# Performance work log

Measured on AMD Instinct MI355X. Metric: run time of the kernel, lower is better.

The kernel has to match this reference:

```python
import jax, jax.numpy as jnp
import numpy as np

B, L, D, NH, NV, T = 4096, 5, 128, 16, 4, 100
NUM_USERS = NUM_ITEMS = 100000
FC1_DIM = NV * D + NH * sum(L - l + 1 for l in range(1, L + 1))  # 752


def setup_inputs() -> dict:
    key = jax.random.key(0)
    ks = jax.random.split(key, 12)
    s = 0.02
    return {
        "seq": jax.random.randint(ks[0], (B, L), 0, NUM_ITEMS),
        "user": jax.random.randint(ks[1], (B,), 0, NUM_USERS),
        "items": jax.random.randint(ks[2], (B, T), 0, NUM_ITEMS),
        "item_table": jax.random.normal(ks[3], (NUM_ITEMS, D), jnp.float32) * s,
        "user_table": jax.random.normal(ks[4], (NUM_USERS, D), jnp.float32) * s,
        "Wv": jax.random.normal(ks[5], (NV, L), jnp.float32) * s,
        "bv": jnp.zeros((NV,), jnp.float32),
        "Wh": jax.random.normal(ks[6], (L, NH, L, D), jnp.float32) * s,
        "bh": jnp.zeros((L, NH), jnp.float32),
        "W1": jax.random.normal(ks[7], (FC1_DIM, D), jnp.float32) * s,
        "b1": jnp.zeros((D,), jnp.float32),
        "W2_table": jax.random.normal(ks[8], (NUM_ITEMS, 2 * D), jnp.float32) * s,
        "b2_table": jnp.zeros((NUM_ITEMS, 1), jnp.float32),
        "_predict": 1,
    }


def reference(seq, user, items, item_table, user_table, Wv, bv, Wh, bh, W1, b1, W2_table, b2_table, _predict):
    emb = item_table[seq]            # (B, L, D)
    uemb = user_table[user]          # (B, D)

    # vertical conv: kernel (L,1), nv out channels -> (B, NV, D), flattened
    ver = jnp.einsum("btd,vt->bvd", emb, Wv) + bv[None, :, None]
    ver_flat = ver.reshape(B, NV * D)

    # horizontal convs: for each kernel length l, NH filters of shape (l, D)
    hor = []
    for l in range(1, L + 1):
        lout = L - l + 1
        # windows: (B, lout, l, D) built from l shifted views
        win = jnp.stack([emb[:, s:s + lout] for s in range(l)], axis=2)
        h = jnp.einsum("btsd,fsd->bft", win, Wh[l - 1, :, :l]) + bh[l - 1][None, :, None]
        hor.append(jax.nn.relu(h).reshape(B, NH * lout))

    z = jnp.concatenate([ver_flat] + hor, axis=1)      # (B, FC1_DIM)
    x = jax.nn.relu(z @ W1 + b1)                        # (B, D)
    xc = jnp.concatenate([x, uemb], axis=1)             # (B, 2D)

    w2 = W2_table[items]                                # (B, T, 2D)
    b2 = b2_table[items][..., 0]                        # (B, T)
    res = jnp.einsum("btd,bd->bt", w2, xc) + b2
    return res
```

## Files before the change

### kernel.cpp

```cpp
#include <hip/hip_runtime.h>


constexpr int Bsz  = 4096;
constexpr int Lq   = 5;
constexpr int Dd   = 128;
constexpr int NHh  = 16;
constexpr int NVv  = 4;
constexpr int Tt   = 100;
constexpr int FC1  = 752;
constexpr int G    = 4;
constexpr int NTHR = 256;

__global__ __launch_bounds__(NTHR, 4) void caser_fused(
    const int* __restrict__ seq, const int* __restrict__ user,
    const int* __restrict__ items,
    const float* __restrict__ item_table, const float* __restrict__ user_table,
    const float* __restrict__ Wv, const float* __restrict__ bv,
    const float* __restrict__ Wh, const float* __restrict__ bh,
    const float* __restrict__ W1, const float* __restrict__ b1,
    const float* __restrict__ W2_table, const float* __restrict__ b2_table,
    float* __restrict__ out)
{
    __shared__ float emb[G][Lq * Dd];
    __shared__ float z[G][FC1];
    __shared__ float xc[G][2 * Dd];
    __shared__ int   s_items[G * Tt];
    __shared__ float s_b2[G * Tt];
    __shared__ float s_res[G * Tt];

    const int tid = threadIdx.x;
    const int b0  = blockIdx.x * G;

    for (int idx = tid; idx < G * Tt; idx += NTHR) {
        int it = items[b0 * Tt + idx];
        s_items[idx] = it;
        s_b2[idx]    = b2_table[it];
    }

    for (int idx = tid; idx < G * Lq * Dd; idx += NTHR) {
        int gt  = idx >> 7;
        int d   = idx & (Dd - 1);
        int row = seq[b0 * Lq + gt];
        emb[0][idx] = item_table[row * Dd + d];
    }
    for (int idx = tid; idx < G * Dd; idx += NTHR) {
        int g = idx >> 7, d = idx & (Dd - 1);
        xc[g][Dd + d] = user_table[user[b0 + g] * Dd + d];
    }
    __syncthreads();

    for (int idx = tid; idx < G * NVv * Dd; idx += NTHR) {
        int g = idx >> 9;
        int v = (idx >> 7) & 3;
        int d = idx & (Dd - 1);
        float acc = bv[v];
        #pragma unroll
        for (int t = 0; t < Lq; ++t)
            acc = fmaf(emb[g][t * Dd + d], Wv[v * Lq + t], acc);
        z[g][v * Dd + d] = acc;
    }

    if (tid < 240) {
        int glt = tid >> 4, f = tid & 15;
        int l, t;
        if      (glt < 5)  { l = 1; t = glt; }
        else if (glt < 9)  { l = 2; t = glt - 5; }
        else if (glt < 12) { l = 3; t = glt - 9; }
        else if (glt < 14) { l = 4; t = glt - 12; }
        else               { l = 5; t = 0; }
        const int lout = Lq - l + 1;
        const int zoff = (l == 1) ? 0 : (l == 2) ? 80 : (l == 3) ? 144
                       : (l == 4) ? 192 : 224;
        float acc[G];
        {
            float bias = bh[(l - 1) * NHh + f];
            #pragma unroll
            for (int g = 0; g < G; ++g) acc[g] = bias;
        }
        for (int s = 0; s < l; ++s) {
            const float4* w4 = reinterpret_cast<const float4*>(
                Wh + (((l - 1) * NHh + f) * Lq + s) * Dd);
            const int ebase = (t + s) * Dd;
            #pragma unroll 4
            for (int d4 = 0; d4 < Dd / 4; ++d4) {
                float4 w = w4[d4];
                #pragma unroll
                for (int g = 0; g < G; ++g) {
                    float4 e = *reinterpret_cast<const float4*>(
                        &emb[g][ebase + d4 * 4]);
                    acc[g] = fmaf(e.x, w.x,
                             fmaf(e.y, w.y,
                             fmaf(e.z, w.z,
                             fmaf(e.w, w.w, acc[g]))));
                }
            }
        }
        #pragma unroll
        for (int g = 0; g < G; ++g)
            z[g][NVv * Dd + zoff + f * lout + t] = fmaxf(acc[g], 0.0f);
    }
    __syncthreads();

    float* part = &emb[0][0];
    {
        int j = tid & (Dd - 1);
        int half = tid >> 7;
        float acc[G] = {0.f, 0.f, 0.f, 0.f};
        const float* w1p = W1 + j;
        int i0 = half * (FC1 / 2);
        for (int i = i0; i < i0 + FC1 / 2; i += 4) {
            float4 zz[G];
            #pragma unroll
            for (int g = 0; g < G; ++g)
                zz[g] = *reinterpret_cast<const float4*>(&z[g][i]);
            float w0 = w1p[(i + 0) * Dd];
            float w1 = w1p[(i + 1) * Dd];
            float w2 = w1p[(i + 2) * Dd];
            float w3 = w1p[(i + 3) * Dd];
            #pragma unroll
            for (int g = 0; g < G; ++g)
                acc[g] = fmaf(zz[g].x, w0,
                         fmaf(zz[g].y, w1,
                         fmaf(zz[g].z, w2,
                         fmaf(zz[g].w, w3, acc[g]))));
        }
        #pragma unroll
        for (int g = 0; g < G; ++g)
            part[(half * G + g) * Dd + j] = acc[g];
    }
    __syncthreads();
    if (tid < Dd) {
        #pragma unroll
        for (int g = 0; g < G; ++g)
            xc[g][tid] = fmaxf(part[g * Dd + tid] + part[(G + g) * Dd + tid]
                               + b1[tid], 0.0f);
    }
    __syncthreads();

    {
        const int g    = tid >> 6;
        const int lane = tid & 63;
        const float4 xf = reinterpret_cast<const float4*>(&xc[g][0])[lane];
        #pragma unroll 4
        for (int t = 0; t < Tt; ++t) {
            const float4* wp = reinterpret_cast<const float4*>(
                W2_table + s_items[g * Tt + t] * (2 * Dd));
            float4 w = wp[lane];
            float v = fmaf(w.x, xf.x,
                      fmaf(w.y, xf.y,
                      fmaf(w.z, xf.z, w.w * xf.w)));
            #pragma unroll
            for (int off = 32; off; off >>= 1)
                v += __shfl_xor(v, off);
            if (lane == 0) s_res[g * Tt + t] = v + s_b2[g * Tt + t];
        }
    }
    __syncthreads();
    for (int idx = tid; idx < G * Tt; idx += NTHR)
        out[b0 * Tt + idx] = s_res[idx];
}

extern "C" void kernel_launch(void* const* d_in, const int* in_sizes, int n_in,
                              void* d_out, int out_size, void* d_ws, size_t ws_size,
                              hipStream_t stream) {
    const int*   seq        = (const int*)  d_in[0];
    const int*   user       = (const int*)  d_in[1];
    const int*   items      = (const int*)  d_in[2];
    const float* item_table = (const float*)d_in[3];
    const float* user_table = (const float*)d_in[4];
    const float* Wv         = (const float*)d_in[5];
    const float* bv         = (const float*)d_in[6];
    const float* Wh         = (const float*)d_in[7];
    const float* bh         = (const float*)d_in[8];
    const float* W1         = (const float*)d_in[9];
    const float* b1         = (const float*)d_in[10];
    const float* W2_table   = (const float*)d_in[11];
    const float* b2_table   = (const float*)d_in[12];
    float* out = (float*)d_out;

    caser_fused<<<dim3(Bsz / G), dim3(NTHR), 0, stream>>>(
        seq, user, items, item_table, user_table, Wv, bv, Wh, bh,
        W1, b1, W2_table, b2_table, out);
}
```

Measured before the change: 337.9 us.

## Split fused kernel into front MLP kernel and per-row scoring tail kernel

Splits the single fused kernel into two launches. The first computes the conv and FC1 features and writes the concatenated user vector to workspace. The second launches one block per batch row, with four waves each scoring a quarter of the items. The aim is more parallelism and memory-level concurrency for the W2_table gather, which was serialized per wave in the fused version. The cost is an extra launch and a global round-trip for the xc vectors.

```diff
diff --git a/kernel.cpp b/kernel.cpp
--- a/kernel.cpp
+++ b/kernel.cpp
@@ -11,31 +11,20 @@
 constexpr int G    = 4;
 constexpr int NTHR = 256;
 
-__global__ __launch_bounds__(NTHR, 4) void caser_fused(
+__global__ __launch_bounds__(NTHR, 4) void caser_front(
     const int* __restrict__ seq, const int* __restrict__ user,
-    const int* __restrict__ items,
     const float* __restrict__ item_table, const float* __restrict__ user_table,
     const float* __restrict__ Wv, const float* __restrict__ bv,
     const float* __restrict__ Wh, const float* __restrict__ bh,
     const float* __restrict__ W1, const float* __restrict__ b1,
-    const float* __restrict__ W2_table, const float* __restrict__ b2_table,
-    float* __restrict__ out)
+    float* __restrict__ xc_ws)
 {
     __shared__ float emb[G][Lq * Dd];
     __shared__ float z[G][FC1];
     __shared__ float xc[G][2 * Dd];
-    __shared__ int   s_items[G * Tt];
-    __shared__ float s_b2[G * Tt];
-    __shared__ float s_res[G * Tt];
 
     const int tid = threadIdx.x;
     const int b0  = blockIdx.x * G;
-
-    for (int idx = tid; idx < G * Tt; idx += NTHR) {
-        int it = items[b0 * Tt + idx];
-        s_items[idx] = it;
-        s_b2[idx]    = b2_table[it];
-    }
 
     for (int idx = tid; idx < G * Lq * Dd; idx += NTHR) {
         int gt  = idx >> 7;
@@ -137,27 +126,46 @@
     }
     __syncthreads();
 
-    {
-        const int g    = tid >> 6;
-        const int lane = tid & 63;
-        const float4 xf = reinterpret_cast<const float4*>(&xc[g][0])[lane];
-        #pragma unroll 4
-        for (int t = 0; t < Tt; ++t) {
-            const float4* wp = reinterpret_cast<const float4*>(
-                W2_table + s_items[g * Tt + t] * (2 * Dd));
-            float4 w = wp[lane];
-            float v = fmaf(w.x, xf.x,
-                      fmaf(w.y, xf.y,
-                      fmaf(w.z, xf.z, w.w * xf.w)));
-            #pragma unroll
-            for (int off = 32; off; off >>= 1)
-                v += __shfl_xor(v, off);
-            if (lane == 0) s_res[g * Tt + t] = v + s_b2[g * Tt + t];
-        }
+    for (int idx = tid; idx < G * 2 * Dd; idx += NTHR)
+        xc_ws[b0 * 2 * Dd + idx] = xc[0][idx];
+}
+
+__global__ __launch_bounds__(NTHR, 8) void caser_tail(
+    const int* __restrict__ items,
+    const float* __restrict__ W2_table, const float* __restrict__ b2_table,
+    const float* __restrict__ xc_ws, float* __restrict__ out)
+{
+    __shared__ int   s_items[Tt];
+    __shared__ float s_b2[Tt];
+
+    const int b    = blockIdx.x;
+    const int tid  = threadIdx.x;
+    const int lane = tid & 63;
+    const int wv   = tid >> 6;
+
+    if (tid < Tt) {
+        int it = items[b * Tt + tid];
+        s_items[tid] = it;
+        s_b2[tid]    = b2_table[it];
     }
+    const float4 xf =
+        reinterpret_cast<const float4*>(xc_ws + b * 2 * Dd)[lane];
     __syncthreads();
-    for (int idx = tid; idx < G * Tt; idx += NTHR)
-        out[b0 * Tt + idx] = s_res[idx];
+
+    #pragma unroll 4
+    for (int k = 0; k < Tt / 4; ++k) {
+        const int t = wv + k * 4;
+        const float4* wp = reinterpret_cast<const float4*>(
+            W2_table + (size_t)s_items[t] * (2 * Dd));
+        float4 w = wp[lane];
+        float v = fmaf(w.x, xf.x,
+                  fmaf(w.y, xf.y,
+                  fmaf(w.z, xf.z, w.w * xf.w)));
+        #pragma unroll
+        for (int off = 32; off; off >>= 1)
+            v += __shfl_xor(v, off);
+        if (lane == 0) out[b * Tt + t] = v + s_b2[t];
+    }
 }
 
 extern "C" void kernel_launch(void* const* d_in, const int* in_sizes, int n_in,
@@ -176,9 +184,11 @@
     const float* b1         = (const float*)d_in[10];
     const float* W2_table   = (const float*)d_in[11];
     const float* b2_table   = (const float*)d_in[12];
-    float* out = (float*)d_out;
+    float* out   = (float*)d_out;
+    float* xc_ws = (float*)d_ws;
 
-    caser_fused<<<dim3(Bsz / G), dim3(NTHR), 0, stream>>>(
-        seq, user, items, item_table, user_table, Wv, bv, Wh, bh,
-        W1, b1, W2_table, b2_table, out);
+    caser_front<<<dim3(Bsz / G), dim3(NTHR), 0, stream>>>(
+        seq, user, item_table, user_table, Wv, bv, Wh, bh, W1, b1, xc_ws);
+    caser_tail<<<dim3(Bsz), dim3(NTHR), 0, stream>>>(
+        items, W2_table, b2_table, xc_ws, out);
 }
```

Measured after the change: 325.6 us. -3.6%, faster.
